# Optimization experiments

Hardware: AMD Instinct MI355X
Metric: run time of the kernel (lower is better)

Reference implementation:

```python
import jax, jax.numpy as jnp
import numpy as np

EPS = 1e-5


def _bn(x, g, b, m, v):
    # eval-mode BatchNorm over the last (channel) axis
    return g * (x - m) * jax.lax.rsqrt(v + EPS) + b


def setup_inputs() -> dict:
    key = jax.random.key(0)
    ks = jax.random.split(key, 16)
    B, N, K, C, Cout, G = 2, 16384, 32, 64, 64, 10
    inp = {
        "points": jax.random.normal(ks[0], (B, N, 3), jnp.float32),
        "features": jax.random.normal(ks[1], (B, N, C), jnp.float32),
        "grouped_idx": jax.random.randint(ks[2], (B, N, K), 0, N, jnp.int32),
        # pos_proj: Conv2d(geo_ch, in_ch, 1) + BN + ReLU
        "W_pos": jax.random.normal(ks[3], (C, G), jnp.float32) / np.sqrt(G),
        "b_pos": jnp.zeros((C,), jnp.float32),
        "bn1_g": jnp.ones((C,), jnp.float32),
        "bn1_b": jnp.zeros((C,), jnp.float32),
        "bn1_m": jax.random.normal(ks[4], (C,), jnp.float32) * 0.1,
        "bn1_v": jax.random.uniform(ks[5], (C,), jnp.float32, 0.5, 1.5),
        # gcm_layer: Conv2d(in_ch, in_ch, 1) + BN + ReLU
        "W_gcm": jax.random.normal(ks[6], (C, C), jnp.float32) / np.sqrt(C),
        "b_gcm": jnp.zeros((C,), jnp.float32),
        "bn2_g": jnp.ones((C,), jnp.float32),
        "bn2_b": jnp.zeros((C,), jnp.float32),
        "bn2_m": jax.random.normal(ks[7], (C,), jnp.float32) * 0.1,
        "bn2_v": jax.random.uniform(ks[8], (C,), jnp.float32, 0.5, 1.5),
        # att_conv_catfea: Linear(nsample, 1)
        "W_att": jax.random.normal(ks[9], (K,), jnp.float32) / np.sqrt(K),
        "b_att": jnp.zeros((), jnp.float32),
        # out_layer: Linear(in_ch, out_ch) + LayerNorm + ReLU
        "W_out": jax.random.normal(ks[10], (Cout, C), jnp.float32) / np.sqrt(C),
        "b_out": jnp.zeros((Cout,), jnp.float32),
        "ln_g": jnp.ones((Cout,), jnp.float32),
        "ln_b": jnp.zeros((Cout,), jnp.float32),
    }
    return inp


def reference(points, features, grouped_idx, W_pos, b_pos, bn1_g, bn1_b, bn1_m, bn1_v,
              W_gcm, b_gcm, bn2_g, bn2_b, bn2_m, bn2_v, W_att, b_att,
              W_out, b_out, ln_g, ln_b):
    gather = jax.vmap(lambda arr, idx: arr[idx])  # [N,C],[N,K] -> [N,K,C]
    grouped_points = gather(points, grouped_idx)          # [B,N,K,3]
    grouped_f = gather(features, grouped_idx)             # [B,N,K,C]

    # legacy geometric encoding: [xi, xj, xi - xj, ||xi - xj||] -> geo_ch = 10
    xi = points[:, :, None, :]
    diff = xi - grouped_points
    dist = jnp.linalg.norm(diff, axis=-1, keepdims=True)
    geo = jnp.concatenate(
        [jnp.broadcast_to(xi, grouped_points.shape), grouped_points, diff, dist], axis=-1)

    # pos_proj: 1x1 conv == channel linear, + BN + ReLU
    expanded = jax.nn.relu(_bn(jnp.einsum('bnkg,cg->bnkc', geo, W_pos) + b_pos,
                               bn1_g, bn1_b, bn1_m, bn1_v))

    h = grouped_f + expanded
    # gcm_layer
    h = jax.nn.relu(_bn(jnp.einsum('bnkc,dc->bnkd', h, W_gcm) + b_gcm,
                        bn2_g, bn2_b, bn2_m, bn2_v))

    # attention over neighbor dim K -> score per channel, softmax over channels (dim=2 of [B,N,C,1])
    score = jnp.einsum('bnkc,k->bnc', h, W_att) + b_att   # [B,N,C]
    score = jax.nn.softmax(score, axis=-1)
    h = h * score[:, :, None, :]                          # [B,N,K,C]

    pooled = jnp.max(h, axis=2)                           # maxpooling downsample -> [B,N,C]
    res = pooled + features

    # out_layer: Linear + LayerNorm + ReLU
    y = jnp.einsum('bnc,oc->bno', res, W_out) + b_out
    mu = jnp.mean(y, axis=-1, keepdims=True)
    var = jnp.var(y, axis=-1, keepdims=True)
    y = ln_g * (y - mu) * jax.lax.rsqrt(var + EPS) + ln_b
    return jax.nn.relu(y)
```

## Files before the change

kernel.cpp:

```cpp
#include <hip/hip_runtime.h>
#include <hip/hip_bf16.h>

#define EPSF 1e-5f

typedef __attribute__((ext_vector_type(8))) short bf16x8;
typedef __attribute__((ext_vector_type(4))) float f32x4;
typedef __attribute__((ext_vector_type(2))) unsigned int u32x2;
typedef __attribute__((ext_vector_type(4))) unsigned int u32x4;

constexpr int B_ = 2, N_ = 16384;
constexpr int HSTR = 72;
constexpr int RSTR = 72;
constexpr int PPW  = 4;
constexpr int PPB  = 16;
constexpr size_t PP_BYTES = (size_t)B_ * N_ * 16;

__device__ __forceinline__ short f2bf(float f) {
    __hip_bfloat16 h = __float2bfloat16(f);
    short s; __builtin_memcpy(&s, &h, 2); return s;
}
__device__ __forceinline__ unsigned int pkbf(float a, float b) {
    float2 f2; f2.x = a; f2.y = b;
    __hip_bfloat162 h = __float22bfloat162_rn(f2);
    unsigned int u; __builtin_memcpy(&u, &h, 4); return u;
}

__global__ __launch_bounds__(256) void prep_points(
    const float* __restrict__ pts, float* __restrict__ pp)
{
    const int i = blockIdx.x * 256 + threadIdx.x;
    if (i < B_ * N_) {
        f32x4 o = { pts[3 * i], pts[3 * i + 1], pts[3 * i + 2], 0.f };
        ((f32x4*)pp)[i] = o;
    }
}

template<bool PAD>
__global__ __launch_bounds__(256) void bridgenet6(
    const float* __restrict__ points,
    const float* __restrict__ pp,
    const float* __restrict__ features,
    const int*   __restrict__ gidx,
    const float* __restrict__ Wpos,
    const float* __restrict__ bposv,
    const float* __restrict__ bn1g, const float* __restrict__ bn1b,
    const float* __restrict__ bn1m, const float* __restrict__ bn1v,
    const float* __restrict__ Wgcm,
    const float* __restrict__ bgcm,
    const float* __restrict__ bn2g, const float* __restrict__ bn2b,
    const float* __restrict__ bn2m, const float* __restrict__ bn2v,
    const float* __restrict__ Watt,
    const float* __restrict__ batt,
    const float* __restrict__ Wout,
    const float* __restrict__ bout,
    const float* __restrict__ lng, const float* __restrict__ lnb,
    float* __restrict__ out)
{
    __shared__ __align__(16) short hbuf[4][32 * HSTR];
    __shared__ __align__(16) short resstage[PPB * RSTR];
    __shared__ __align__(16) short wb2[8 * 64 * 8];
    __shared__ __align__(16) short wb3[8 * 64 * 8];

    const int t    = threadIdx.x;
    const int w    = t >> 6;
    const int l    = t & 63;
    const int l15  = l & 15;
    const int quad = l >> 4;
    const int c4   = l15 * 4;

    if (w == 0) {
        #pragma unroll
        for (int nt = 0; nt < 4; ++nt)
            #pragma unroll
            for (int ks = 0; ks < 2; ++ks) {
                bf16x8 f2, f3;
                #pragma unroll
                for (int j = 0; j < 8; ++j) {
                    f2[j] = f2bf(Wgcm[(c4 + nt) * 64 + ks * 32 + quad * 8 + j]);
                    f3[j] = f2bf(Wout[(c4 + nt) * 64 + ks * 32 + quad * 8 + j]);
                }
                *(bf16x8*)&wb2[((nt * 2 + ks) * 64 + l) * 8] = f2;
                *(bf16x8*)&wb3[((nt * 2 + ks) * 64 + l) * 8] = f3;
            }
    }

    bf16x8 bposf[4];
    #pragma unroll
    for (int nt = 0; nt < 4; ++nt) {
        const int c = c4 + nt;
        #pragma unroll
        for (int j = 0; j < 8; ++j) {
            const int g = quad * 8 + j;
            bposf[nt][j] = f2bf(g < 10 ? Wpos[c * 10 + g] : 0.f);
        }
    }
    f32x4 ps1, pb1, ps2, pb2;
    {
        const f32x4 g1 = *(const f32x4*)(bn1g + c4);
        const f32x4 b1 = *(const f32x4*)(bn1b + c4);
        const f32x4 m1 = *(const f32x4*)(bn1m + c4);
        const f32x4 v1 = *(const f32x4*)(bn1v + c4);
        const f32x4 bp = *(const f32x4*)(bposv + c4);
        const f32x4 g2 = *(const f32x4*)(bn2g + c4);
        const f32x4 b2 = *(const f32x4*)(bn2b + c4);
        const f32x4 m2 = *(const f32x4*)(bn2m + c4);
        const f32x4 v2 = *(const f32x4*)(bn2v + c4);
        const f32x4 bg = *(const f32x4*)(bgcm + c4);
        #pragma unroll
        for (int j = 0; j < 4; ++j) {
            ps1[j] = g1[j] * rsqrtf(v1[j] + EPSF);
            pb1[j] = ps1[j] * (bp[j] - m1[j]) + b1[j];
            ps2[j] = g2[j] * rsqrtf(v2[j] + EPSF);
            pb2[j] = ps2[j] * (bg[j] - m2[j]) + b2[j];
        }
    }
    float wat[2][4];
    #pragma unroll
    for (int mt = 0; mt < 2; ++mt)
        #pragma unroll
        for (int r = 0; r < 4; ++r)
            wat[mt][r] = Watt[mt * 16 + quad * 4 + r];
    const float battv = batt[0];

    const f32x4 zero4 = {0.f, 0.f, 0.f, 0.f};
    short* hb = hbuf[w];
    const int base = blockIdx.x * PPB + w * PPW;
    const int bb   = (base >> 14) * N_;

    __syncthreads();

    for (int i = 0; i < PPW; ++i) {
        const int pt = base + i;

        int giv[2];
        giv[0] = gidx[(size_t)pt * 32 + l15];
        giv[1] = gidx[(size_t)pt * 32 + 16 + l15];
        const f32x4 resid = *(const f32x4*)(features + (size_t)pt * 64 + c4);
        float xi0, xi1, xi2;
        float px[2], py[2], pz[2];
        if (PAD) {
            const f32x4 x4 = *(const f32x4*)(pp + (size_t)pt * 4);
            xi0 = x4[0]; xi1 = x4[1]; xi2 = x4[2];
            #pragma unroll
            for (int mt = 0; mt < 2; ++mt) {
                const f32x4 p4 = *(const f32x4*)(pp + (size_t)(bb + giv[mt]) * 4);
                px[mt] = p4[0]; py[mt] = p4[1]; pz[mt] = p4[2];
            }
        } else {
            xi0 = points[(size_t)pt * 3];
            xi1 = points[(size_t)pt * 3 + 1];
            xi2 = points[(size_t)pt * 3 + 2];
            #pragma unroll
            for (int mt = 0; mt < 2; ++mt) {
                const float* ppt = points + (size_t)(bb + giv[mt]) * 3;
                px[mt] = ppt[0]; py[mt] = ppt[1]; pz[mt] = ppt[2];
            }
        }
        f32x4 f4[2][4];
        #pragma unroll
        for (int mt = 0; mt < 2; ++mt)
            #pragma unroll
            for (int r = 0; r < 4; ++r) {
                const int gs = __shfl(giv[mt], quad * 4 + r);
                f4[mt][r] = *(const f32x4*)(features + (size_t)(bb + gs) * 64 + c4);
            }

        bf16x8 ageo[2];
        #pragma unroll
        for (int mt = 0; mt < 2; ++mt) {
            const float dx = xi0 - px[mt], dy = xi1 - py[mt], dz = xi2 - pz[mt];
            const float dist = sqrtf(dx * dx + dy * dy + dz * dz);
            u32x4 u = {0u, 0u, 0u, 0u};
            if (quad == 0) {
                u[0] = pkbf(xi0, xi1); u[1] = pkbf(xi2, px[mt]);
                u[2] = pkbf(py[mt], pz[mt]); u[3] = pkbf(dx, dy);
            } else if (quad == 1) {
                u[0] = pkbf(dz, dist);
            }
            __builtin_memcpy(&ageo[mt], &u, 16);
        }

        f32x4 acc1[2][4];
        #pragma unroll
        for (int mt = 0; mt < 2; ++mt)
            #pragma unroll
            for (int nt = 0; nt < 4; ++nt)
                acc1[mt][nt] = __builtin_amdgcn_mfma_f32_16x16x32_bf16(
                    ageo[mt], bposf[nt], zero4, 0, 0, 0);

        #pragma unroll
        for (int mt = 0; mt < 2; ++mt)
            #pragma unroll
            for (int r = 0; r < 4; ++r) {
                const int k = mt * 16 + quad * 4 + r;
                float v[4];
                #pragma unroll
                for (int j = 0; j < 4; ++j)
                    v[j] = f4[mt][r][j] + fmaxf(ps1[j] * acc1[mt][j][r] + pb1[j], 0.f);
                u32x2 hv = { pkbf(v[0], v[1]), pkbf(v[2], v[3]) };
                *(u32x2*)&hb[k * HSTR + c4] = hv;
            }

        bf16x8 a2[2][2];
        #pragma unroll
        for (int mt = 0; mt < 2; ++mt)
            #pragma unroll
            for (int ks = 0; ks < 2; ++ks)
                a2[mt][ks] = *(const bf16x8*)&hb[(mt * 16 + l15) * HSTR + ks * 32 + quad * 8];
        f32x4 acc2[2][4];
        #pragma unroll
        for (int nt = 0; nt < 4; ++nt) {
            const bf16x8 b0 = *(const bf16x8*)&wb2[((nt * 2 + 0) * 64 + l) * 8];
            const bf16x8 b1 = *(const bf16x8*)&wb2[((nt * 2 + 1) * 64 + l) * 8];
            #pragma unroll
            for (int mt = 0; mt < 2; ++mt) {
                f32x4 a = __builtin_amdgcn_mfma_f32_16x16x32_bf16(a2[mt][0], b0, zero4, 0, 0, 0);
                acc2[mt][nt] = __builtin_amdgcn_mfma_f32_16x16x32_bf16(a2[mt][1], b1, a, 0, 0, 0);
            }
        }

        float res[4];
        {
            float sp[4], mk[4];
            #pragma unroll
            for (int nt = 0; nt < 4; ++nt) {
                sp[nt] = 0.f; mk[nt] = 0.f;
                #pragma unroll
                for (int mt = 0; mt < 2; ++mt)
                    #pragma unroll
                    for (int r = 0; r < 4; ++r) {
                        const float h2 = fmaxf(ps2[nt] * acc2[mt][nt][r] + pb2[nt], 0.f);
                        sp[nt] += h2 * wat[mt][r];
                        mk[nt] = fmaxf(mk[nt], h2);
                    }
                sp[nt] += __shfl_xor(sp[nt], 16);
                sp[nt] += __shfl_xor(sp[nt], 32);
                mk[nt] = fmaxf(mk[nt], __shfl_xor(mk[nt], 16));
                mk[nt] = fmaxf(mk[nt], __shfl_xor(mk[nt], 32));
            }
            float e[4], s = 0.f;
            #pragma unroll
            for (int nt = 0; nt < 4; ++nt) { e[nt] = __expf(sp[nt] + battv); s += e[nt]; }
            #pragma unroll
            for (int o = 1; o < 16; o <<= 1) s += __shfl_xor(s, o);
            const float inv = 1.f / s;
            #pragma unroll
            for (int nt = 0; nt < 4; ++nt)
                res[nt] = e[nt] * inv * mk[nt] + resid[nt];
        }
        if (quad == 0) {
            u32x2 rv = { pkbf(res[0], res[1]), pkbf(res[2], res[3]) };
            *(u32x2*)&resstage[(w * PPW + i) * RSTR + c4] = rv;
        }
    }

    __syncthreads();

    const f32x4 lngv  = *(const f32x4*)(lng + c4);
    const f32x4 lnbv  = *(const f32x4*)(lnb + c4);
    const f32x4 boutv = *(const f32x4*)(bout + c4);
    bf16x8 a3[2];
    #pragma unroll
    for (int ks = 0; ks < 2; ++ks)
        a3[ks] = *(const bf16x8*)&resstage[l15 * RSTR + ks * 32 + quad * 8];
    f32x4 acc3[4];
    #pragma unroll
    for (int nt = 0; nt < 4; ++nt) {
        const bf16x8 b0 = *(const bf16x8*)&wb3[((nt * 2 + 0) * 64 + l) * 8];
        const bf16x8 b1 = *(const bf16x8*)&wb3[((nt * 2 + 1) * 64 + l) * 8];
        f32x4 a = __builtin_amdgcn_mfma_f32_16x16x32_bf16(a3[0], b0, zero4, 0, 0, 0);
        acc3[nt] = __builtin_amdgcn_mfma_f32_16x16x32_bf16(a3[1], b1, a, 0, 0, 0);
    }
    float y[4], s = 0.f;
    #pragma unroll
    for (int nt = 0; nt < 4; ++nt) { y[nt] = acc3[nt][w] + boutv[nt]; s += y[nt]; }
    #pragma unroll
    for (int o = 1; o < 16; o <<= 1) s += __shfl_xor(s, o);
    const float mu = s * (1.f / 64.f);
    float dv[4], v2 = 0.f;
    #pragma unroll
    for (int nt = 0; nt < 4; ++nt) { dv[nt] = y[nt] - mu; v2 += dv[nt] * dv[nt]; }
    #pragma unroll
    for (int o = 1; o < 16; o <<= 1) v2 += __shfl_xor(v2, o);
    const float rs = rsqrtf(v2 * (1.f / 64.f) + EPSF);
    const int pto = blockIdx.x * PPB + quad * 4 + w;
    f32x4 ov;
    #pragma unroll
    for (int nt = 0; nt < 4; ++nt)
        ov[nt] = fmaxf(lngv[nt] * dv[nt] * rs + lnbv[nt], 0.f);
    *(f32x4*)(out + (size_t)pto * 64 + c4) = ov;
}

extern "C" void kernel_launch(void* const* d_in, const int* in_sizes, int n_in,
                              void* d_out, int out_size, void* d_ws, size_t ws_size,
                              hipStream_t stream) {
    const float* points   = (const float*)d_in[0];
    const float* features = (const float*)d_in[1];
    const int*   gidxp    = (const int*)d_in[2];
    const bool   pad      = (ws_size >= PP_BYTES);
    float* pp = (float*)d_ws;
    if (pad) {
        hipLaunchKernelGGL(prep_points, dim3((B_ * N_ + 255) / 256), dim3(256), 0, stream,
                           points, pp);
        hipLaunchKernelGGL((bridgenet6<true>), dim3((B_ * N_) / PPB), dim3(256), 0, stream,
            points, pp, features, gidxp,
            (const float*)d_in[3],  (const float*)d_in[4],
            (const float*)d_in[5],  (const float*)d_in[6],  (const float*)d_in[7],  (const float*)d_in[8],
            (const float*)d_in[9],  (const float*)d_in[10],
            (const float*)d_in[11], (const float*)d_in[12], (const float*)d_in[13], (const float*)d_in[14],
            (const float*)d_in[15], (const float*)d_in[16],
            (const float*)d_in[17], (const float*)d_in[18],
            (const float*)d_in[19], (const float*)d_in[20],
            (float*)d_out);
    } else {
        hipLaunchKernelGGL((bridgenet6<false>), dim3((B_ * N_) / PPB), dim3(256), 0, stream,
            points, pp, features, gidxp,
            (const float*)d_in[3],  (const float*)d_in[4],
            (const float*)d_in[5],  (const float*)d_in[6],  (const float*)d_in[7],  (const float*)d_in[8],
            (const float*)d_in[9],  (const float*)d_in[10],
            (const float*)d_in[11], (const float*)d_in[12], (const float*)d_in[13], (const float*)d_in[14],
            (const float*)d_in[15], (const float*)d_in[16],
            (const float*)d_in[17], (const float*)d_in[18],
            (const float*)d_in[19], (const float*)d_in[20],
            (float*)d_out);
    }
}
```

Before: 174.6 us.

## Prefetch neighbor indices, remap blocks across XCDs, drop Wout LDS staging

Neighbor indices for the next point are loaded one iteration ahead as int4 vectors, so the feature gathers no longer wait on a shuffle and a dependent index load. Block IDs are remapped so that interleaved workgroups, which likely land on different XCDs, cover contiguous ranges within each batch. The Wgcm staging into LDS is now split across all four waves using vector loads. Wout is read from global memory straight into registers instead of through an LDS buffer. This cuts serial latency and LDS use, at the cost of extra registers and repeated per-wave global reads of Wout.

```diff
diff --git a/kernel.cpp b/kernel.cpp
--- a/kernel.cpp
+++ b/kernel.cpp
@@ -7,6 +7,7 @@
 typedef __attribute__((ext_vector_type(4))) float f32x4;
 typedef __attribute__((ext_vector_type(2))) unsigned int u32x2;
 typedef __attribute__((ext_vector_type(4))) unsigned int u32x4;
+typedef __attribute__((ext_vector_type(4))) int i32x4;
 
 constexpr int B_ = 2, N_ = 16384;
 constexpr int HSTR = 72;
@@ -36,7 +37,7 @@
 }
 
 template<bool PAD>
-__global__ __launch_bounds__(256) void bridgenet6(
+__global__ __launch_bounds__(256) void bridgenet7(
     const float* __restrict__ points,
     const float* __restrict__ pp,
     const float* __restrict__ features,
@@ -59,7 +60,6 @@
     __shared__ __align__(16) short hbuf[4][32 * HSTR];
     __shared__ __align__(16) short resstage[PPB * RSTR];
     __shared__ __align__(16) short wb2[8 * 64 * 8];
-    __shared__ __align__(16) short wb3[8 * 64 * 8];
 
     const int t    = threadIdx.x;
     const int w    = t >> 6;
@@ -68,20 +68,25 @@
     const int quad = l >> 4;
     const int c4   = l15 * 4;
 
-    if (w == 0) {
-        #pragma unroll
-        for (int nt = 0; nt < 4; ++nt)
-            #pragma unroll
-            for (int ks = 0; ks < 2; ++ks) {
-                bf16x8 f2, f3;
-                #pragma unroll
-                for (int j = 0; j < 8; ++j) {
-                    f2[j] = f2bf(Wgcm[(c4 + nt) * 64 + ks * 32 + quad * 8 + j]);
-                    f3[j] = f2bf(Wout[(c4 + nt) * 64 + ks * 32 + quad * 8 + j]);
-                }
-                *(bf16x8*)&wb2[((nt * 2 + ks) * 64 + l) * 8] = f2;
-                *(bf16x8*)&wb3[((nt * 2 + ks) * 64 + l) * 8] = f3;
-            }
+    const int wg  = blockIdx.x;
+    const int blk = ((wg & 7) >> 2) * 1024 + (wg >> 3) * 4 + (wg & 3);
+
+    {
+        #pragma unroll
+        for (int u = 0; u < 2; ++u) {
+            const int s  = w * 2 + u;
+            const int nt = s >> 1, ks = s & 1;
+            const float* g = Wgcm + (c4 + nt) * 64 + ks * 32 + quad * 8;
+            const f32x4 w0 = *(const f32x4*)g;
+            const f32x4 w1 = *(const f32x4*)(g + 4);
+            bf16x8 f2;
+            #pragma unroll
+            for (int j = 0; j < 4; ++j) {
+                f2[j]     = f2bf(w0[j]);
+                f2[j + 4] = f2bf(w1[j]);
+            }
+            *(bf16x8*)&wb2[(s * 64 + l) * 8] = f2;
+        }
     }
 
     bf16x8 bposf[4];
@@ -124,17 +129,28 @@
 
     const f32x4 zero4 = {0.f, 0.f, 0.f, 0.f};
     short* hb = hbuf[w];
-    const int base = blockIdx.x * PPB + w * PPW;
-    const int bb   = (base >> 14) * N_;
+    const int base = blk * PPB + w * PPW;
+    const int bb   = (blk >> 10) * N_;
+
+    i32x4 gi4[2];
+    int   giv[2];
+    gi4[0] = *(const i32x4*)(gidx + (size_t)base * 32 + quad * 4);
+    gi4[1] = *(const i32x4*)(gidx + (size_t)base * 32 + 16 + quad * 4);
+    giv[0] = gidx[(size_t)base * 32 + l15];
+    giv[1] = gidx[(size_t)base * 32 + 16 + l15];
 
     __syncthreads();
 
     for (int i = 0; i < PPW; ++i) {
         const int pt = base + i;
 
-        int giv[2];
-        giv[0] = gidx[(size_t)pt * 32 + l15];
-        giv[1] = gidx[(size_t)pt * 32 + 16 + l15];
+        f32x4 f4[2][4];
+        #pragma unroll
+        for (int mt = 0; mt < 2; ++mt)
+            #pragma unroll
+            for (int r = 0; r < 4; ++r)
+                f4[mt][r] = *(const f32x4*)(features + (size_t)(bb + gi4[mt][r]) * 64 + c4);
+
         const f32x4 resid = *(const f32x4*)(features + (size_t)pt * 64 + c4);
         float xi0, xi1, xi2;
         float px[2], py[2], pz[2];
@@ -156,14 +172,14 @@
                 px[mt] = ppt[0]; py[mt] = ppt[1]; pz[mt] = ppt[2];
             }
         }
-        f32x4 f4[2][4];
-        #pragma unroll
-        for (int mt = 0; mt < 2; ++mt)
-            #pragma unroll
-            for (int r = 0; r < 4; ++r) {
-                const int gs = __shfl(giv[mt], quad * 4 + r);
-                f4[mt][r] = *(const f32x4*)(features + (size_t)(bb + gs) * 64 + c4);
-            }
+
+        const int ptn = base + (i + 1 < PPW ? i + 1 : i);
+        i32x4 ngi[2];
+        int   ngiv[2];
+        ngi[0]  = *(const i32x4*)(gidx + (size_t)ptn * 32 + quad * 4);
+        ngi[1]  = *(const i32x4*)(gidx + (size_t)ptn * 32 + 16 + quad * 4);
+        ngiv[0] = gidx[(size_t)ptn * 32 + l15];
+        ngiv[1] = gidx[(size_t)ptn * 32 + 16 + l15];
 
         bf16x8 ageo[2];
         #pragma unroll
@@ -252,6 +268,9 @@
             u32x2 rv = { pkbf(res[0], res[1]), pkbf(res[2], res[3]) };
             *(u32x2*)&resstage[(w * PPW + i) * RSTR + c4] = rv;
         }
+
+        gi4[0] = ngi[0]; gi4[1] = ngi[1];
+        giv[0] = ngiv[0]; giv[1] = ngiv[1];
     }
 
     __syncthreads();
@@ -266,8 +285,19 @@
     f32x4 acc3[4];
     #pragma unroll
     for (int nt = 0; nt < 4; ++nt) {
-        const bf16x8 b0 = *(const bf16x8*)&wb3[((nt * 2 + 0) * 64 + l) * 8];
-        const bf16x8 b1 = *(const bf16x8*)&wb3[((nt * 2 + 1) * 64 + l) * 8];
+        const float* g = Wout + (c4 + nt) * 64 + quad * 8;
+        const f32x4 w00 = *(const f32x4*)g;
+        const f32x4 w01 = *(const f32x4*)(g + 4);
+        const f32x4 w10 = *(const f32x4*)(g + 32);
+        const f32x4 w11 = *(const f32x4*)(g + 36);
+        bf16x8 b0, b1;
+        #pragma unroll
+        for (int j = 0; j < 4; ++j) {
+            b0[j]     = f2bf(w00[j]);
+            b0[j + 4] = f2bf(w01[j]);
+            b1[j]     = f2bf(w10[j]);
+            b1[j + 4] = f2bf(w11[j]);
+        }
         f32x4 a = __builtin_amdgcn_mfma_f32_16x16x32_bf16(a3[0], b0, zero4, 0, 0, 0);
         acc3[nt] = __builtin_amdgcn_mfma_f32_16x16x32_bf16(a3[1], b1, a, 0, 0, 0);
     }
@@ -283,7 +313,7 @@
     #pragma unroll
     for (int o = 1; o < 16; o <<= 1) v2 += __shfl_xor(v2, o);
     const float rs = rsqrtf(v2 * (1.f / 64.f) + EPSF);
-    const int pto = blockIdx.x * PPB + quad * 4 + w;
+    const int pto = blk * PPB + quad * 4 + w;
     f32x4 ov;
     #pragma unroll
     for (int nt = 0; nt < 4; ++nt)
@@ -302,7 +332,7 @@
     if (pad) {
         hipLaunchKernelGGL(prep_points, dim3((B_ * N_ + 255) / 256), dim3(256), 0, stream,
                            points, pp);
-        hipLaunchKernelGGL((bridgenet6<true>), dim3((B_ * N_) / PPB), dim3(256), 0, stream,
+        hipLaunchKernelGGL((bridgenet7<true>), dim3((B_ * N_) / PPB), dim3(256), 0, stream,
             points, pp, features, gidxp,
             (const float*)d_in[3],  (const float*)d_in[4],
             (const float*)d_in[5],  (const float*)d_in[6],  (const float*)d_in[7],  (const float*)d_in[8],
@@ -313,7 +343,7 @@
             (const float*)d_in[19], (const float*)d_in[20],
             (float*)d_out);
     } else {
-        hipLaunchKernelGGL((bridgenet6<false>), dim3((B_ * N_) / PPB), dim3(256), 0, stream,
+        hipLaunchKernelGGL((bridgenet7<false>), dim3((B_ * N_) / PPB), dim3(256), 0, stream,
             points, pp, features, gidxp,
             (const float*)d_in[3],  (const float*)d_in[4],
             (const float*)d_in[5],  (const float*)d_in[6],  (const float*)d_in[7],  (const float*)d_in[8],
```

Measured after the change: 183.2 us. 1.05x slower.

## Software-pipeline neighbor gathers across points and remap blocks for XCD locality

Applied to the files above, without the earlier changes.

Prefetches the next point's gathered feature rows and geometry, and the index vector two points ahead, while the current point is processed. This hides the latency of the random gathers behind the MFMA work. Indices are now loaded as vectors, which removes the shuffles, and the weight conversion to bf16 is split across all four waves instead of wave 0. Block IDs are remapped so that neighboring blocks land on the same XCD for cache locality, at the cost of more live registers, which may lower occupancy.

```diff
diff --git a/kernel.cpp b/kernel.cpp
--- a/kernel.cpp
+++ b/kernel.cpp
@@ -7,6 +7,7 @@
 typedef __attribute__((ext_vector_type(4))) float f32x4;
 typedef __attribute__((ext_vector_type(2))) unsigned int u32x2;
 typedef __attribute__((ext_vector_type(4))) unsigned int u32x4;
+typedef __attribute__((ext_vector_type(4))) int i32x4;
 
 constexpr int B_ = 2, N_ = 16384;
 constexpr int HSTR = 72;
@@ -36,7 +37,7 @@
 }
 
 template<bool PAD>
-__global__ __launch_bounds__(256) void bridgenet6(
+__global__ __launch_bounds__(256) void bridgenet8(
     const float* __restrict__ points,
     const float* __restrict__ pp,
     const float* __restrict__ features,
@@ -68,20 +69,26 @@
     const int quad = l >> 4;
     const int c4   = l15 * 4;
 
-    if (w == 0) {
-        #pragma unroll
-        for (int nt = 0; nt < 4; ++nt)
-            #pragma unroll
-            for (int ks = 0; ks < 2; ++ks) {
-                bf16x8 f2, f3;
-                #pragma unroll
-                for (int j = 0; j < 8; ++j) {
-                    f2[j] = f2bf(Wgcm[(c4 + nt) * 64 + ks * 32 + quad * 8 + j]);
-                    f3[j] = f2bf(Wout[(c4 + nt) * 64 + ks * 32 + quad * 8 + j]);
-                }
-                *(bf16x8*)&wb2[((nt * 2 + ks) * 64 + l) * 8] = f2;
-                *(bf16x8*)&wb3[((nt * 2 + ks) * 64 + l) * 8] = f3;
-            }
+    const int wg  = blockIdx.x;
+    const int blk = ((wg & 7) >> 2) * 1024 + (wg >> 3) * 4 + (wg & 3);
+
+    {
+        #pragma unroll
+        for (int u = 0; u < 4; ++u) {
+            const int s  = w * 4 + u;
+            const int nt = (s >> 1) & 3, ks = s & 1;
+            const float* src = (s < 8 ? Wgcm : Wout) + (c4 + nt) * 64 + ks * 32 + quad * 8;
+            const f32x4 w0 = *(const f32x4*)src;
+            const f32x4 w1 = *(const f32x4*)(src + 4);
+            bf16x8 f;
+            #pragma unroll
+            for (int j = 0; j < 4; ++j) {
+                f[j]     = f2bf(w0[j]);
+                f[j + 4] = f2bf(w1[j]);
+            }
+            short* dst = (s < 8 ? wb2 : wb3);
+            *(bf16x8*)&dst[((s & 7) * 64 + l) * 8] = f;
+        }
     }
 
     bf16x8 bposf[4];
@@ -124,26 +131,30 @@
 
     const f32x4 zero4 = {0.f, 0.f, 0.f, 0.f};
     short* hb = hbuf[w];
-    const int base = blockIdx.x * PPB + w * PPW;
-    const int bb   = (base >> 14) * N_;
-
-    __syncthreads();
-
-    for (int i = 0; i < PPW; ++i) {
-        const int pt = base + i;
-
-        int giv[2];
-        giv[0] = gidx[(size_t)pt * 32 + l15];
-        giv[1] = gidx[(size_t)pt * 32 + 16 + l15];
-        const f32x4 resid = *(const f32x4*)(features + (size_t)pt * 64 + c4);
-        float xi0, xi1, xi2;
-        float px[2], py[2], pz[2];
+    const int base = blk * PPB + w * PPW;
+    const int bb   = (blk >> 10) * N_;
+
+    auto LOADI = [&](int pt, i32x4 (&gi)[2]) {
+        gi[0] = *(const i32x4*)(gidx + (size_t)pt * 32 + quad * 4);
+        gi[1] = *(const i32x4*)(gidx + (size_t)pt * 32 + 16 + quad * 4);
+    };
+    auto LOADD = [&](int pt, const i32x4 (&gi)[2],
+                     f32x4 (&f4)[2][4], bf16x8 (&ageo)[2]) {
+        #pragma unroll
+        for (int mt = 0; mt < 2; ++mt)
+            #pragma unroll
+            for (int r = 0; r < 4; ++r)
+                f4[mt][r] = *(const f32x4*)(features + (size_t)(bb + gi[mt][r]) * 64 + c4);
+        int gv[2];
+        gv[0] = gidx[(size_t)pt * 32 + l15];
+        gv[1] = gidx[(size_t)pt * 32 + 16 + l15];
+        float xi0, xi1, xi2, px[2], py[2], pz[2];
         if (PAD) {
             const f32x4 x4 = *(const f32x4*)(pp + (size_t)pt * 4);
             xi0 = x4[0]; xi1 = x4[1]; xi2 = x4[2];
             #pragma unroll
             for (int mt = 0; mt < 2; ++mt) {
-                const f32x4 p4 = *(const f32x4*)(pp + (size_t)(bb + giv[mt]) * 4);
+                const f32x4 p4 = *(const f32x4*)(pp + (size_t)(bb + gv[mt]) * 4);
                 px[mt] = p4[0]; py[mt] = p4[1]; pz[mt] = p4[2];
             }
         } else {
@@ -152,20 +163,10 @@
             xi2 = points[(size_t)pt * 3 + 2];
             #pragma unroll
             for (int mt = 0; mt < 2; ++mt) {
-                const float* ppt = points + (size_t)(bb + giv[mt]) * 3;
+                const float* ppt = points + (size_t)(bb + gv[mt]) * 3;
                 px[mt] = ppt[0]; py[mt] = ppt[1]; pz[mt] = ppt[2];
             }
         }
-        f32x4 f4[2][4];
-        #pragma unroll
-        for (int mt = 0; mt < 2; ++mt)
-            #pragma unroll
-            for (int r = 0; r < 4; ++r) {
-                const int gs = __shfl(giv[mt], quad * 4 + r);
-                f4[mt][r] = *(const f32x4*)(features + (size_t)(bb + gs) * 64 + c4);
-            }
-
-        bf16x8 ageo[2];
         #pragma unroll
         for (int mt = 0; mt < 2; ++mt) {
             const float dx = xi0 - px[mt], dy = xi1 - py[mt], dz = xi2 - pz[mt];
@@ -179,6 +180,28 @@
             }
             __builtin_memcpy(&ageo[mt], &u, 16);
         }
+    };
+
+    i32x4 giC[2], giN[2];
+    LOADI(base, giC);
+    LOADI(base + 1, giN);
+    f32x4  f4c[2][4];
+    bf16x8 ageoc[2];
+    LOADD(base, giC, f4c, ageoc);
+
+    __syncthreads();
+
+    #pragma unroll
+    for (int i = 0; i < PPW; ++i) {
+        const int pt = base + i;
+
+        f32x4  f4n[2][4];
+        bf16x8 ageon[2];
+        i32x4  giN2[2];
+        if (i + 1 < PPW) LOADD(pt + 1, giN, f4n, ageon);
+        if (i + 2 < PPW) LOADI(pt + 2, giN2);
+
+        const f32x4 resid = *(const f32x4*)(features + (size_t)pt * 64 + c4);
 
         f32x4 acc1[2][4];
         #pragma unroll
@@ -186,7 +209,7 @@
             #pragma unroll
             for (int nt = 0; nt < 4; ++nt)
                 acc1[mt][nt] = __builtin_amdgcn_mfma_f32_16x16x32_bf16(
-                    ageo[mt], bposf[nt], zero4, 0, 0, 0);
+                    ageoc[mt], bposf[nt], zero4, 0, 0, 0);
 
         #pragma unroll
         for (int mt = 0; mt < 2; ++mt)
@@ -196,7 +219,7 @@
                 float v[4];
                 #pragma unroll
                 for (int j = 0; j < 4; ++j)
-                    v[j] = f4[mt][r][j] + fmaxf(ps1[j] * acc1[mt][j][r] + pb1[j], 0.f);
+                    v[j] = f4c[mt][r][j] + fmaxf(ps1[j] * acc1[mt][j][r] + pb1[j], 0.f);
                 u32x2 hv = { pkbf(v[0], v[1]), pkbf(v[2], v[3]) };
                 *(u32x2*)&hb[k * HSTR + c4] = hv;
             }
@@ -252,6 +275,16 @@
             u32x2 rv = { pkbf(res[0], res[1]), pkbf(res[2], res[3]) };
             *(u32x2*)&resstage[(w * PPW + i) * RSTR + c4] = rv;
         }
+
+        if (i + 1 < PPW) {
+            #pragma unroll
+            for (int mt = 0; mt < 2; ++mt) {
+                #pragma unroll
+                for (int r = 0; r < 4; ++r) f4c[mt][r] = f4n[mt][r];
+                ageoc[mt] = ageon[mt];
+            }
+            if (i + 2 < PPW) { giN[0] = giN2[0]; giN[1] = giN2[1]; }
+        }
     }
 
     __syncthreads();
@@ -283,7 +316,7 @@
     #pragma unroll
     for (int o = 1; o < 16; o <<= 1) v2 += __shfl_xor(v2, o);
     const float rs = rsqrtf(v2 * (1.f / 64.f) + EPSF);
-    const int pto = blockIdx.x * PPB + quad * 4 + w;
+    const int pto = blk * PPB + quad * 4 + w;
     f32x4 ov;
     #pragma unroll
     for (int nt = 0; nt < 4; ++nt)
@@ -302,7 +335,7 @@
     if (pad) {
         hipLaunchKernelGGL(prep_points, dim3((B_ * N_ + 255) / 256), dim3(256), 0, stream,
                            points, pp);
-        hipLaunchKernelGGL((bridgenet6<true>), dim3((B_ * N_) / PPB), dim3(256), 0, stream,
+        hipLaunchKernelGGL((bridgenet8<true>), dim3((B_ * N_) / PPB), dim3(256), 0, stream,
             points, pp, features, gidxp,
             (const float*)d_in[3],  (const float*)d_in[4],
             (const float*)d_in[5],  (const float*)d_in[6],  (const float*)d_in[7],  (const float*)d_in[8],
@@ -313,7 +346,7 @@
             (const float*)d_in[19], (const float*)d_in[20],
             (float*)d_out);
     } else {
-        hipLaunchKernelGGL((bridgenet6<false>), dim3((B_ * N_) / PPB), dim3(256), 0, stream,
+        hipLaunchKernelGGL((bridgenet8<false>), dim3((B_ * N_) / PPB), dim3(256), 0, stream,
             points, pp, features, gidxp,
             (const float*)d_in[3],  (const float*)d_in[4],
             (const float*)d_in[5],  (const float*)d_in[6],  (const float*)d_in[7],  (const float*)d_in[8],
```

Measured after the change: 180.6 us. 1.03x slower.
